# Performance work log

Measured on AMD Instinct MI355X. Metric: run time of the kernel, lower is better.

Reference implementation:

```python
import jax, jax.numpy as jnp
import numpy as np

# ForwardDiffusion config (init_kwargs)
TMIN, TMAX, DT = 0.0, 1.0, 0.001
LENGTH = 1024
BATCH = 64
THETA = 1.0      # mu(x, t) = -THETA * x   (Ornstein-Uhlenbeck drift)
SIGMA0 = 0.5     # sigma(x, t) = SIGMA0    (constant diffusion)

_TIME = jnp.asarray(np.arange(TMIN, TMAX, DT), dtype=jnp.float32)
STEPS = _TIME.shape[0]  # 1000


def setup_inputs() -> dict:
    key = jax.random.key(0)
    kx, kn = jax.random.split(key)
    x = jax.random.normal(kx, (BATCH, LENGTH), dtype=jnp.float32)
    # per-step noise vector, shape (steps-1, length); broadcast over batch like the
    # original tf.random.normal((length,))
    noise = jax.random.normal(kn, (STEPS - 1, LENGTH), dtype=jnp.float32)
    return {"x": x, "noise": noise}


def reference(x, noise):
    dt = jnp.float32(DT)
    sqrt_dt = jnp.sqrt(dt)

    def mu(x, t):
        return -THETA * x

    def sigma(x, t):
        return jnp.float32(SIGMA0)

    def step(carry, inp):
        t, z = inp  # t: scalar, z: (length,)
        x_new = carry + mu(carry, t) * dt + sigma(carry, t) * sqrt_dt * z
        return x_new, x_new

    # Euler-Maruyama scan over time steps 1..steps-1
    _, xs = jax.lax.scan(step, x, (_TIME[1:], noise))  # xs: [steps-1, batch, length]
    traj = jnp.concatenate([x[None], xs], axis=0)       # [steps, batch, length]
    return jnp.transpose(traj, (1, 0, 2))               # [batch, steps, length]
```

## Files before the change

### kernel.cpp

```cpp
#include <hip/hip_runtime.h>
#include <math.h>


namespace {
constexpr int LEN    = 1024;
constexpr int BATCH  = 64;
constexpr int STEPS  = 1000;
constexpr int NST    = 999;
constexpr int CHUNK  = 16;
constexpr int NCHUNK = (NST + CHUNK - 1) / CHUNK;
constexpr float THETA = 1.0f;
constexpr float DT    = 0.001f;
typedef float f32x4 __attribute__((ext_vector_type(4)));
}

__global__ __launch_bounds__(256) void k_partial(const float* __restrict__ noise,
                                                 float* __restrict__ S) {
    const int l = blockIdx.y * 256 + threadIdx.x;
    const int g = blockIdx.x;
    const float a = 1.0f - THETA * DT;
    if (g == 0) S[l] = 0.0f;
    const int t0 = g * CHUNK + 1;
    const int t1 = min((g + 1) * CHUNK, NST);
    float acc = 0.0f;
    #pragma unroll
    for (int t = t0; t <= t1; ++t) {
        acc = a * acc + noise[(t - 1) * LEN + l];
        S[t * LEN + l] = acc;
    }
}

__global__ __launch_bounds__(256) void k_combine(const float* __restrict__ S,
                                                 float* __restrict__ carry,
                                                 float* __restrict__ apow) {
    const int l = blockIdx.x * 256 + threadIdx.x;
    const float a = 1.0f - THETA * DT;
    if (l < STEPS) apow[l] = powf(a, (float)l);

    float vals[NCHUNK];
    #pragma unroll
    for (int g = 0; g < NCHUNK; ++g) {
        const int t1 = min((g + 1) * CHUNK, NST);
        vals[g] = S[t1 * LEN + l];
    }
    const float a16 = 0.98411684f;
    float cr = 0.0f;
    #pragma unroll
    for (int g = 0; g < NCHUNK; ++g) {
        carry[g * LEN + l] = cr;
        cr = a16 * cr + vals[g];
    }
}

__global__ __launch_bounds__(256) void k_emit(const float* __restrict__ x0,
                                              const float* __restrict__ S,
                                              const float* __restrict__ carry,
                                              const float* __restrict__ apow,
                                              float* __restrict__ out) {
    const int b = blockIdx.x;
    const int g = blockIdx.y;
    const float c = 0.5f * sqrtf(DT);
    const int l4 = threadIdx.x;
    const f32x4 x   = ((const f32x4*)(x0 + b * LEN))[l4];
    const f32x4 ccr = c * ((const f32x4*)(carry + g * LEN))[l4];
    float* outb = out + (size_t)b * STEPS * LEN;

    if (g == 0) {
        __builtin_nontemporal_store(x, (f32x4*)outb + l4);
    }
    const int tbase = g * CHUNK;

    auto emit1 = [&](int i) {
        const int t = tbase + i;
        const float ap  = apow[t];
        const float apl = apow[i];
        const f32x4 s = ((const f32x4*)(S + t * LEN))[l4];
        f32x4 o = ap * x + c * s + apl * ccr;
        __builtin_nontemporal_store(o, (f32x4*)(outb + (size_t)t * LEN) + l4);
    };

    if (tbase + CHUNK <= NST) {
        #pragma unroll
        for (int i = 1; i <= CHUNK; ++i) emit1(i);
    } else {
        #pragma unroll
        for (int i = 1; i <= NST - (NCHUNK - 1) * CHUNK; ++i) emit1(i);
    }
}

extern "C" void kernel_launch(void* const* d_in, const int* in_sizes, int n_in,
                              void* d_out, int out_size, void* d_ws, size_t ws_size,
                              hipStream_t stream) {
    const float* x     = (const float*)d_in[0];
    const float* noise = (const float*)d_in[1];
    float* out = (float*)d_out;
    float* ws  = (float*)d_ws;

    float* S     = ws;
    float* carry = S + STEPS * LEN;
    float* apow  = carry + NCHUNK * LEN;

    hipLaunchKernelGGL(k_partial, dim3(NCHUNK, 4), dim3(256), 0, stream, noise, S);
    hipLaunchKernelGGL(k_combine, dim3(4), dim3(256), 0, stream, S, carry, apow);
    hipLaunchKernelGGL(k_emit, dim3(BATCH, NCHUNK), dim3(256), 0, stream,
                       x, S, carry, apow, out);
}
```

Baseline: 278.8 us.

## Fuse three scan kernels into one cooperative kernel with grid syncs

Replaces the partial-scan, combine and emit kernel launches with a single cooperative kernel of 504 blocks. The phases are separated by grid-wide syncs, and each block emits 8 (batch, chunk) tiles. This removes two kernel launch gaps and their inter-kernel drain. In exchange it adds two grid barriers, a serial combine phase run by only 4 blocks while the others wait, and fewer resident blocks for the store-bound emit phase.

```diff
diff --git a/kernel.cpp b/kernel.cpp
--- a/kernel.cpp
+++ b/kernel.cpp
@@ -1,6 +1,9 @@
 #include <hip/hip_runtime.h>
+#include <hip/hip_cooperative_groups.h>
 #include <math.h>
 
+
+namespace cg = cooperative_groups;
 
 namespace {
 constexpr int LEN    = 1024;
@@ -9,82 +12,88 @@
 constexpr int NST    = 999;
 constexpr int CHUNK  = 16;
 constexpr int NCHUNK = (NST + CHUNK - 1) / CHUNK;
+constexpr int GRID   = 504;
 constexpr float THETA = 1.0f;
 constexpr float DT    = 0.001f;
 typedef float f32x4 __attribute__((ext_vector_type(4)));
 }
 
-__global__ __launch_bounds__(256) void k_partial(const float* __restrict__ noise,
-                                                 float* __restrict__ S) {
-    const int l = blockIdx.y * 256 + threadIdx.x;
-    const int g = blockIdx.x;
+__global__ __launch_bounds__(256, 2) void k_fused(const float* __restrict__ x0,
+                                                  const float* __restrict__ noise,
+                                                  float* __restrict__ S,
+                                                  float* __restrict__ carry,
+                                                  float* __restrict__ apow,
+                                                  float* __restrict__ out) {
+    const int tid = threadIdx.x;
+    const int blk = blockIdx.x;
     const float a = 1.0f - THETA * DT;
-    if (g == 0) S[l] = 0.0f;
-    const int t0 = g * CHUNK + 1;
-    const int t1 = min((g + 1) * CHUNK, NST);
-    float acc = 0.0f;
-    #pragma unroll
-    for (int t = t0; t <= t1; ++t) {
-        acc = a * acc + noise[(t - 1) * LEN + l];
-        S[t * LEN + l] = acc;
+
+    if (blk < NCHUNK * 4) {
+        const int g = blk >> 2;
+        const int l = (blk & 3) * 256 + tid;
+        if (g == 0) S[l] = 0.0f;
+        const int t0 = g * CHUNK + 1;
+        const int t1 = min((g + 1) * CHUNK, NST);
+        float acc = 0.0f;
+        #pragma unroll
+        for (int t = t0; t <= t1; ++t) {
+            acc = a * acc + noise[(t - 1) * LEN + l];
+            S[t * LEN + l] = acc;
+        }
     }
-}
+    cg::this_grid().sync();
 
-__global__ __launch_bounds__(256) void k_combine(const float* __restrict__ S,
-                                                 float* __restrict__ carry,
-                                                 float* __restrict__ apow) {
-    const int l = blockIdx.x * 256 + threadIdx.x;
-    const float a = 1.0f - THETA * DT;
-    if (l < STEPS) apow[l] = powf(a, (float)l);
+    if (blk < 4) {
+        const int l = blk * 256 + tid;
+        if (l < STEPS) apow[l] = powf(a, (float)l);
+        float vals[NCHUNK];
+        #pragma unroll
+        for (int g = 0; g < NCHUNK; ++g) {
+            const int t1 = min((g + 1) * CHUNK, NST);
+            vals[g] = S[t1 * LEN + l];
+        }
+        const float a16 = 0.98411684f;
+        float cr = 0.0f;
+        #pragma unroll
+        for (int g = 0; g < NCHUNK; ++g) {
+            carry[g * LEN + l] = cr;
+            cr = a16 * cr + vals[g];
+        }
+    }
+    cg::this_grid().sync();
 
-    float vals[NCHUNK];
-    #pragma unroll
-    for (int g = 0; g < NCHUNK; ++g) {
-        const int t1 = min((g + 1) * CHUNK, NST);
-        vals[g] = S[t1 * LEN + l];
-    }
-    const float a16 = 0.98411684f;
-    float cr = 0.0f;
-    #pragma unroll
-    for (int g = 0; g < NCHUNK; ++g) {
-        carry[g * LEN + l] = cr;
-        cr = a16 * cr + vals[g];
-    }
-}
+    const float c = 0.5f * sqrtf(DT);
+    #pragma unroll 1
+    for (int it = 0; it < 8; ++it) {
+        const int tile = blk * 8 + it;
+        const int b = tile / NCHUNK;
+        const int g = tile - b * NCHUNK;
+        const int tbase = g * CHUNK;
 
-__global__ __launch_bounds__(256) void k_emit(const float* __restrict__ x0,
-                                              const float* __restrict__ S,
-                                              const float* __restrict__ carry,
-                                              const float* __restrict__ apow,
-                                              float* __restrict__ out) {
-    const int b = blockIdx.x;
-    const int g = blockIdx.y;
-    const float c = 0.5f * sqrtf(DT);
-    const int l4 = threadIdx.x;
-    const f32x4 x   = ((const f32x4*)(x0 + b * LEN))[l4];
-    const f32x4 ccr = c * ((const f32x4*)(carry + g * LEN))[l4];
-    float* outb = out + (size_t)b * STEPS * LEN;
+        const f32x4 x   = ((const f32x4*)(x0 + b * LEN))[tid];
+        const f32x4 ccr = c * ((const f32x4*)(carry + g * LEN))[tid];
+        float* outb = out + (size_t)b * STEPS * LEN;
 
-    if (g == 0) {
-        __builtin_nontemporal_store(x, (f32x4*)outb + l4);
-    }
-    const int tbase = g * CHUNK;
+        if (g == 0) {
+            __builtin_nontemporal_store(x, (f32x4*)outb + tid);
+        }
 
-    auto emit1 = [&](int i) {
-        const int t = tbase + i;
-        const float ap  = apow[t];
-        const float apl = apow[i];
-        const f32x4 s = ((const f32x4*)(S + t * LEN))[l4];
-        f32x4 o = ap * x + c * s + apl * ccr;
-        __builtin_nontemporal_store(o, (f32x4*)(outb + (size_t)t * LEN) + l4);
-    };
+        auto emit1 = [&](int i) {
+            const int t = tbase + i;
+            const float ap  = apow[t];
+            const float apl = apow[i];
+            const f32x4 s = ((const f32x4*)(S + (size_t)t * LEN))[tid];
+            f32x4 o = ap * x + c * s + apl * ccr;
+            __builtin_nontemporal_store(o, (f32x4*)(outb + (size_t)t * LEN) + tid);
+        };
 
-    if (tbase + CHUNK <= NST) {
-        #pragma unroll
-        for (int i = 1; i <= CHUNK; ++i) emit1(i);
-    } else {
-        #pragma unroll
-        for (int i = 1; i <= NST - (NCHUNK - 1) * CHUNK; ++i) emit1(i);
+        if (g != NCHUNK - 1) {
+            #pragma unroll
+            for (int i = 1; i <= CHUNK; ++i) emit1(i);
+        } else {
+            #pragma unroll
+            for (int i = 1; i <= NST - (NCHUNK - 1) * CHUNK; ++i) emit1(i);
+        }
     }
 }
 
@@ -100,8 +109,8 @@
     float* carry = S + STEPS * LEN;
     float* apow  = carry + NCHUNK * LEN;
 
-    hipLaunchKernelGGL(k_partial, dim3(NCHUNK, 4), dim3(256), 0, stream, noise, S);
-    hipLaunchKernelGGL(k_combine, dim3(4), dim3(256), 0, stream, S, carry, apow);
-    hipLaunchKernelGGL(k_emit, dim3(BATCH, NCHUNK), dim3(256), 0, stream,
-                       x, S, carry, apow, out);
+    void* args[] = {(void*)&x, (void*)&noise, (void*)&S, (void*)&carry,
+                    (void*)&apow, (void*)&out};
+    hipLaunchCooperativeKernel((const void*)k_fused, dim3(GRID), dim3(256),
+                               args, 0, stream);
 }
```

Result: slower. 404.0 us (+44.9%).
